# Kernel optimization log

Hardware: AMD Instinct MI355X
Metric: run time of the kernel (lower is better)

The kernel has to match this reference:

```python
import jax, jax.numpy as jnp
import numpy as np

H = 1024
B = 8192

def setup_inputs() -> dict:
    key = jax.random.key(0)
    ks = jax.random.split(key, 8)
    s = 1.0 / np.sqrt(H)
    return {
        "x": jax.random.normal(ks[0], (B, H), jnp.float32),
        "h": jax.random.normal(ks[1], (B, H), jnp.float32),
        "W_ih_w": jax.random.normal(ks[2], (3 * H, H), jnp.float32) * s,
        "W_ih_b": jax.random.normal(ks[3], (3 * H,), jnp.float32) * s,
        "U_r_w": jax.random.normal(ks[4], (H, H), jnp.float32) * s,
        "U_z_w": jax.random.normal(ks[5], (H, H), jnp.float32) * s,
        "U_n_w": jax.random.normal(ks[6], (H, H), jnp.float32) * s,
        "U_n_b": jax.random.normal(ks[7], (H,), jnp.float32) * s,
    }

def reference(x, h, W_ih_w, W_ih_b, U_r_w, U_z_w, U_n_w, U_n_b):
    # fused input projection: (B, 3H)
    x_proj = x @ W_ih_w.T + W_ih_b
    r_x, z_x, n_x = jnp.split(x_proj, 3, axis=-1)
    # per-gate hidden matmuls (transpose_U=False path)
    r_h = h @ U_r_w.T
    z_h = h @ U_z_w.T
    n_h = h @ U_n_w.T + U_n_b
    r = jax.nn.sigmoid(r_x + r_h)
    z = jax.nn.sigmoid(z_x + z_h)
    n = jnp.tanh(n_x + r * n_h)
    return (1.0 - z) * n + z * h
```

## Files before the change

kernel.cpp:

```cpp
#include <hip/hip_runtime.h>
#include <hip/hip_bf16.h>
#include <cstdint>

#define HDIM 1024
#define BM 128
#define BN 64
#define BKK 32

typedef __attribute__((ext_vector_type(8))) __bf16 bf16x8;
typedef __attribute__((ext_vector_type(8))) unsigned short u16x8;
typedef __attribute__((ext_vector_type(4))) float f32x4;

static __device__ __forceinline__ unsigned short f2b(float f) {
    __hip_bfloat16 h = __float2bfloat16(f);
    return __builtin_bit_cast(unsigned short, h);
}

__global__ void __launch_bounds__(256) cvt_kernel(const float* __restrict__ src,
                                                  unsigned short* __restrict__ dst,
                                                  int n4) {
    int i = blockIdx.x * blockDim.x + threadIdx.x;
    if (i >= n4) return;
    float4 v = ((const float4*)src)[i];
    ushort4 o;
    o.x = f2b(v.x); o.y = f2b(v.y); o.z = f2b(v.z); o.w = f2b(v.w);
    ((ushort4*)dst)[i] = o;
}

__global__ void __launch_bounds__(256, 2)
gru_fused(const float* __restrict__ xg, const float* __restrict__ hg,
          const unsigned short* __restrict__ wih,
          const unsigned short* __restrict__ ur,
          const unsigned short* __restrict__ uz,
          const unsigned short* __restrict__ un,
          const float* __restrict__ bih, const float* __restrict__ bun,
          float* __restrict__ out) {
    __shared__ __align__(16) unsigned short smem[20480];
    unsigned short* xs  = smem;
    unsigned short* hs  = smem + 4096;
    unsigned short* wsm = smem + 8192;

    const int tid  = threadIdx.x;
    const int lane = tid & 63;
    const int wv   = tid >> 6;
    const int wm   = wv >> 1;
    const int wn   = wv & 1;
    const int lr   = lane & 15;
    const int ls   = lane >> 4;
    const int m0   = blockIdx.y * BM;
    const int n0   = blockIdx.x * BN;

    const unsigned short* wb[6] = {
        wih + (size_t)n0 * HDIM,
        wih + (size_t)(HDIM + n0) * HDIM,
        wih + (size_t)(2 * HDIM + n0) * HDIM,
        ur  + (size_t)n0 * HDIM,
        uz  + (size_t)n0 * HDIM,
        un  + (size_t)n0 * HDIM
    };

    f32x4 acc[4][4][2];
#pragma unroll
    for (int g = 0; g < 4; ++g)
#pragma unroll
        for (int mf = 0; mf < 4; ++mf)
#pragma unroll
            for (int nf = 0; nf < 2; ++nf)
                acc[g][mf][nf] = f32x4{0.f, 0.f, 0.f, 0.f};

    for (int kt = 0; kt < HDIM / BKK; ++kt) {
        const int k0 = kt * BKK;

        {
            const int c  = wv * 64 + lane;
            const int r  = c >> 2;
            const int sl = c & 3;
#pragma unroll
            for (int mi = 0; mi < 6; ++mi) {
                const unsigned short* g = wb[mi] + (size_t)r * HDIM + k0 + sl * 8;
                unsigned short* l = wsm + mi * 2048 + wv * 512;
                __builtin_amdgcn_global_load_lds(
                    (const __attribute__((address_space(1))) void*)g,
                    (__attribute__((address_space(3))) void*)l, 16, 0, 0);
            }
        }

#pragma unroll
        for (int half = 0; half < 2; ++half) {
            const int ci = tid + half * 256;
            const int r  = ci >> 2;
            const int sl = ci & 3;
            const float* gx = xg + (size_t)(m0 + r) * HDIM + k0 + sl * 8;
            const float* gh = hg + (size_t)(m0 + r) * HDIM + k0 + sl * 8;
            float4 x0 = ((const float4*)gx)[0];
            float4 x1 = ((const float4*)gx)[1];
            float4 h0 = ((const float4*)gh)[0];
            float4 h1 = ((const float4*)gh)[1];
            u16x8 px, ph;
            px[0] = f2b(x0.x); px[1] = f2b(x0.y); px[2] = f2b(x0.z); px[3] = f2b(x0.w);
            px[4] = f2b(x1.x); px[5] = f2b(x1.y); px[6] = f2b(x1.z); px[7] = f2b(x1.w);
            ph[0] = f2b(h0.x); ph[1] = f2b(h0.y); ph[2] = f2b(h0.z); ph[3] = f2b(h0.w);
            ph[4] = f2b(h1.x); ph[5] = f2b(h1.y); ph[6] = f2b(h1.z); ph[7] = f2b(h1.w);
            *(u16x8*)(xs + ci * 8) = px;
            *(u16x8*)(hs + ci * 8) = ph;
        }

        __syncthreads();

        bf16x8 ax[4], ah[4];
#pragma unroll
        for (int mf = 0; mf < 4; ++mf) {
            ax[mf] = *(const bf16x8*)(xs + (wm * 64 + mf * 16 + lr) * 32 + ls * 8);
            ah[mf] = *(const bf16x8*)(hs + (wm * 64 + mf * 16 + lr) * 32 + ls * 8);
        }
#pragma unroll
        for (int mi = 0; mi < 6; ++mi) {
            const unsigned short* wt = wsm + mi * 2048;
            bf16x8 b0 = *(const bf16x8*)(wt + (wn * 32 + lr) * 32 + ls * 8);
            bf16x8 b1 = *(const bf16x8*)(wt + (wn * 32 + 16 + lr) * 32 + ls * 8);
            const int g = (mi == 0 || mi == 3) ? 0 : (mi == 1 || mi == 4) ? 1 : (mi == 2) ? 2 : 3;
            const bf16x8* a = (mi < 3) ? ax : ah;
#pragma unroll
            for (int mf = 0; mf < 4; ++mf) {
                acc[g][mf][0] = __builtin_amdgcn_mfma_f32_16x16x32_bf16(a[mf], b0, acc[g][mf][0], 0, 0, 0);
                acc[g][mf][1] = __builtin_amdgcn_mfma_f32_16x16x32_bf16(a[mf], b1, acc[g][mf][1], 0, 0, 0);
            }
        }
        __syncthreads();
    }

#pragma unroll
    for (int mf = 0; mf < 4; ++mf) {
#pragma unroll
        for (int nf = 0; nf < 2; ++nf) {
            const int gc = n0 + wn * 32 + nf * 16 + lr;
            const float br  = bih[gc];
            const float bz  = bih[HDIM + gc];
            const float bnx = bih[2 * HDIM + gc];
            const float bn2 = bun[gc];
            const f32x4 aR = acc[0][mf][nf];
            const f32x4 aZ = acc[1][mf][nf];
            const f32x4 aX = acc[2][mf][nf];
            const f32x4 aH = acc[3][mf][nf];
#pragma unroll
            for (int rr = 0; rr < 4; ++rr) {
                const int gr = m0 + wm * 64 + mf * 16 + ls * 4 + rr;
                const float rv = 1.f / (1.f + __expf(-(aR[rr] + br)));
                const float zv = 1.f / (1.f + __expf(-(aZ[rr] + bz)));
                const float nv = tanhf(aX[rr] + bnx + rv * (aH[rr] + bn2));
                const float hv = hg[(size_t)gr * HDIM + gc];
                out[(size_t)gr * HDIM + gc] = (1.f - zv) * nv + zv * hv;
            }
        }
    }
}

extern "C" void kernel_launch(void* const* d_in, const int* in_sizes, int n_in,
                              void* d_out, int out_size, void* d_ws, size_t ws_size,
                              hipStream_t stream) {
    const float* x   = (const float*)d_in[0];
    const float* h   = (const float*)d_in[1];
    const float* Wih = (const float*)d_in[2];
    const float* bih = (const float*)d_in[3];
    const float* Ur  = (const float*)d_in[4];
    const float* Uz  = (const float*)d_in[5];
    const float* Un  = (const float*)d_in[6];
    const float* bun = (const float*)d_in[7];
    float* out = (float*)d_out;

    unsigned short* wsp  = (unsigned short*)d_ws;
    unsigned short* wihb = wsp;
    unsigned short* urb  = wihb + 3 * 1024 * 1024;
    unsigned short* uzb  = urb + 1024 * 1024;
    unsigned short* unb  = uzb + 1024 * 1024;

    cvt_kernel<<<3072, 256, 0, stream>>>(Wih, wihb, 3 * 1024 * 1024 / 4);
    cvt_kernel<<<1024, 256, 0, stream>>>(Ur, urb, 1024 * 1024 / 4);
    cvt_kernel<<<1024, 256, 0, stream>>>(Uz, uzb, 1024 * 1024 / 4);
    cvt_kernel<<<1024, 256, 0, stream>>>(Un, unb, 1024 * 1024 / 4);

    dim3 grid(HDIM / BN, 8192 / BM);
    gru_fused<<<grid, 256, 0, stream>>>(x, h, wihb, urb, uzb, unb, bih, bun, out);
}
```

Before: 159.6 us.

## Double-buffer LDS tiles with XOR swizzle and pre-convert activations to bf16

```diff
diff --git a/kernel.cpp b/kernel.cpp
--- a/kernel.cpp
+++ b/kernel.cpp
@@ -6,6 +6,7 @@
 #define BM 128
 #define BN 64
 #define BKK 32
+#define NT (HDIM / BKK)
 
 typedef __attribute__((ext_vector_type(8))) __bf16 bf16x8;
 typedef __attribute__((ext_vector_type(8))) unsigned short u16x8;
@@ -16,29 +17,46 @@
     return __builtin_bit_cast(unsigned short, h);
 }
 
-__global__ void __launch_bounds__(256) cvt_kernel(const float* __restrict__ src,
-                                                  unsigned short* __restrict__ dst,
-                                                  int n4) {
-    int i = blockIdx.x * blockDim.x + threadIdx.x;
-    if (i >= n4) return;
+static __device__ __forceinline__ void barrier_fence() {
+    asm volatile("" ::: "memory");
+    __builtin_amdgcn_s_barrier();
+    asm volatile("" ::: "memory");
+}
+
+__global__ void __launch_bounds__(256) cvt_all(
+    const float* __restrict__ x, const float* __restrict__ h,
+    const float* __restrict__ wih, const float* __restrict__ ur,
+    const float* __restrict__ uz, const float* __restrict__ un,
+    unsigned short* __restrict__ wb, unsigned short* __restrict__ urb,
+    unsigned short* __restrict__ uzb, unsigned short* __restrict__ unb,
+    unsigned short* __restrict__ xb, unsigned short* __restrict__ hb) {
+    int b = blockIdx.x;
+    const float* src; unsigned short* dst; int idx;
+    if (b < 3072)       { src = wih; dst = wb;  idx = b; }
+    else if (b < 4096)  { src = ur;  dst = urb; idx = b - 3072; }
+    else if (b < 5120)  { src = uz;  dst = uzb; idx = b - 4096; }
+    else if (b < 6144)  { src = un;  dst = unb; idx = b - 5120; }
+    else if (b < 14336) { src = x;   dst = xb;  idx = b - 6144; }
+    else                { src = h;   dst = hb;  idx = b - 14336; }
+    int i = idx * 256 + threadIdx.x;
     float4 v = ((const float4*)src)[i];
     ushort4 o;
     o.x = f2b(v.x); o.y = f2b(v.y); o.z = f2b(v.z); o.w = f2b(v.w);
     ((ushort4*)dst)[i] = o;
 }
 
+template<bool XHB>
 __global__ void __launch_bounds__(256, 2)
-gru_fused(const float* __restrict__ xg, const float* __restrict__ hg,
+gru_fused(const float* __restrict__ hg,
+          const unsigned short* __restrict__ xb, const unsigned short* __restrict__ hb,
+          const float* __restrict__ xg32, const float* __restrict__ hg32,
           const unsigned short* __restrict__ wih,
           const unsigned short* __restrict__ ur,
           const unsigned short* __restrict__ uz,
           const unsigned short* __restrict__ un,
           const float* __restrict__ bih, const float* __restrict__ bun,
           float* __restrict__ out) {
-    __shared__ __align__(16) unsigned short smem[20480];
-    unsigned short* xs  = smem;
-    unsigned short* hs  = smem + 4096;
-    unsigned short* wsm = smem + 8192;
+    __shared__ __align__(16) unsigned short smem[2][20480];
 
     const int tid  = threadIdx.x;
     const int lane = tid & 63;
@@ -50,7 +68,7 @@
     const int m0   = blockIdx.y * BM;
     const int n0   = blockIdx.x * BN;
 
-    const unsigned short* wb[6] = {
+    const unsigned short* wb6[6] = {
         wih + (size_t)n0 * HDIM,
         wih + (size_t)(HDIM + n0) * HDIM,
         wih + (size_t)(2 * HDIM + n0) * HDIM,
@@ -59,6 +77,9 @@
         un  + (size_t)n0 * HDIM
     };
 
+    const int wr  = tid >> 2;
+    const int wsl = (tid & 3) ^ ((tid >> 3) & 3);
+
     f32x4 acc[4][4][2];
 #pragma unroll
     for (int g = 0; g < 4; ++g)
@@ -68,56 +89,85 @@
             for (int nf = 0; nf < 2; ++nf)
                 acc[g][mf][nf] = f32x4{0.f, 0.f, 0.f, 0.f};
 
-    for (int kt = 0; kt < HDIM / BKK; ++kt) {
+    auto STAGE = [&](int bufi, int kt) {
         const int k0 = kt * BKK;
-
-        {
-            const int c  = wv * 64 + lane;
-            const int r  = c >> 2;
-            const int sl = c & 3;
-#pragma unroll
-            for (int mi = 0; mi < 6; ++mi) {
-                const unsigned short* g = wb[mi] + (size_t)r * HDIM + k0 + sl * 8;
-                unsigned short* l = wsm + mi * 2048 + wv * 512;
+        unsigned short* sb = &smem[bufi][0];
+        float4 fx[2][2], fh[2][2];
+        if constexpr (!XHB) {
+#pragma unroll
+            for (int half = 0; half < 2; ++half) {
+                const int c2 = half * 256 + tid;
+                const int r2 = c2 >> 2;
+                const int sl = c2 & 3;
+                const float* gx = xg32 + (size_t)(m0 + r2) * HDIM + k0 + sl * 8;
+                const float* gh = hg32 + (size_t)(m0 + r2) * HDIM + k0 + sl * 8;
+                fx[half][0] = ((const float4*)gx)[0];
+                fx[half][1] = ((const float4*)gx)[1];
+                fh[half][0] = ((const float4*)gh)[0];
+                fh[half][1] = ((const float4*)gh)[1];
+            }
+        }
+#pragma unroll
+        for (int mi = 0; mi < 6; ++mi) {
+            const unsigned short* g = wb6[mi] + (size_t)wr * HDIM + k0 + wsl * 8;
+            __builtin_amdgcn_global_load_lds(
+                (const __attribute__((address_space(1))) void*)g,
+                (__attribute__((address_space(3))) void*)(sb + 8192 + mi * 2048 + wv * 512),
+                16, 0, 0);
+        }
+        if constexpr (XHB) {
+#pragma unroll
+            for (int half = 0; half < 2; ++half) {
+                const int c2 = half * 256 + tid;
+                const int r2 = c2 >> 2;
+                const int sl = (c2 & 3) ^ ((c2 >> 3) & 3);
+                const unsigned short* gx = xb + (size_t)(m0 + r2) * HDIM + k0 + sl * 8;
+                const unsigned short* gh = hb + (size_t)(m0 + r2) * HDIM + k0 + sl * 8;
                 __builtin_amdgcn_global_load_lds(
-                    (const __attribute__((address_space(1))) void*)g,
-                    (__attribute__((address_space(3))) void*)l, 16, 0, 0);
-            }
-        }
-
-#pragma unroll
-        for (int half = 0; half < 2; ++half) {
-            const int ci = tid + half * 256;
-            const int r  = ci >> 2;
-            const int sl = ci & 3;
-            const float* gx = xg + (size_t)(m0 + r) * HDIM + k0 + sl * 8;
-            const float* gh = hg + (size_t)(m0 + r) * HDIM + k0 + sl * 8;
-            float4 x0 = ((const float4*)gx)[0];
-            float4 x1 = ((const float4*)gx)[1];
-            float4 h0 = ((const float4*)gh)[0];
-            float4 h1 = ((const float4*)gh)[1];
-            u16x8 px, ph;
-            px[0] = f2b(x0.x); px[1] = f2b(x0.y); px[2] = f2b(x0.z); px[3] = f2b(x0.w);
-            px[4] = f2b(x1.x); px[5] = f2b(x1.y); px[6] = f2b(x1.z); px[7] = f2b(x1.w);
-            ph[0] = f2b(h0.x); ph[1] = f2b(h0.y); ph[2] = f2b(h0.z); ph[3] = f2b(h0.w);
-            ph[4] = f2b(h1.x); ph[5] = f2b(h1.y); ph[6] = f2b(h1.z); ph[7] = f2b(h1.w);
-            *(u16x8*)(xs + ci * 8) = px;
-            *(u16x8*)(hs + ci * 8) = ph;
-        }
-
-        __syncthreads();
-
+                    (const __attribute__((address_space(1))) void*)gx,
+                    (__attribute__((address_space(3))) void*)(sb + half * 2048 + wv * 512),
+                    16, 0, 0);
+                __builtin_amdgcn_global_load_lds(
+                    (const __attribute__((address_space(1))) void*)gh,
+                    (__attribute__((address_space(3))) void*)(sb + 4096 + half * 2048 + wv * 512),
+                    16, 0, 0);
+            }
+        } else {
+#pragma unroll
+            for (int half = 0; half < 2; ++half) {
+                const int c2 = half * 256 + tid;
+                const int r2 = c2 >> 2;
+                const int sp = (c2 & 3) ^ ((c2 >> 3) & 3);
+                u16x8 px, ph;
+#pragma unroll
+                for (int q = 0; q < 4; ++q) {
+                    px[q]     = f2b(fx[half][0][q]);
+                    px[q + 4] = f2b(fx[half][1][q]);
+                    ph[q]     = f2b(fh[half][0][q]);
+                    ph[q + 4] = f2b(fh[half][1][q]);
+                }
+                *(u16x8*)(sb + r2 * 32 + sp * 8)        = px;
+                *(u16x8*)(sb + 4096 + r2 * 32 + sp * 8) = ph;
+            }
+        }
+    };
+
+    auto COMPUTE = [&](int bufi) {
+        const unsigned short* sb = &smem[bufi][0];
+        const int sel = (lr >> 1) & 3;
+        const int fo  = (ls ^ sel) << 3;
         bf16x8 ax[4], ah[4];
 #pragma unroll
         for (int mf = 0; mf < 4; ++mf) {
-            ax[mf] = *(const bf16x8*)(xs + (wm * 64 + mf * 16 + lr) * 32 + ls * 8);
-            ah[mf] = *(const bf16x8*)(hs + (wm * 64 + mf * 16 + lr) * 32 + ls * 8);
+            const int row = wm * 64 + mf * 16 + lr;
+            ax[mf] = *(const bf16x8*)(sb + row * 32 + fo);
+            ah[mf] = *(const bf16x8*)(sb + 4096 + row * 32 + fo);
         }
 #pragma unroll
         for (int mi = 0; mi < 6; ++mi) {
-            const unsigned short* wt = wsm + mi * 2048;
-            bf16x8 b0 = *(const bf16x8*)(wt + (wn * 32 + lr) * 32 + ls * 8);
-            bf16x8 b1 = *(const bf16x8*)(wt + (wn * 32 + 16 + lr) * 32 + ls * 8);
+            const unsigned short* wt = sb + 8192 + mi * 2048;
+            bf16x8 b0 = *(const bf16x8*)(wt + (wn * 32 + lr) * 32 + fo);
+            bf16x8 b1 = *(const bf16x8*)(wt + (wn * 32 + 16 + lr) * 32 + fo);
             const int g = (mi == 0 || mi == 3) ? 0 : (mi == 1 || mi == 4) ? 1 : (mi == 2) ? 2 : 3;
             const bf16x8* a = (mi < 3) ? ax : ah;
 #pragma unroll
@@ -126,18 +176,37 @@
                 acc[g][mf][1] = __builtin_amdgcn_mfma_f32_16x16x32_bf16(a[mf], b1, acc[g][mf][1], 0, 0, 0);
             }
         }
-        __syncthreads();
+    };
+
+    auto WAITN = [&]() {
+        if constexpr (XHB) asm volatile("s_waitcnt vmcnt(10)" ::: "memory");
+        else               asm volatile("s_waitcnt vmcnt(6) lgkmcnt(0)" ::: "memory");
+    };
+
+    STAGE(0, 0);
+#pragma unroll 1
+    for (int kt = 0; kt < NT - 2; kt += 2) {
+        STAGE(1, kt + 1); WAITN(); barrier_fence();
+        COMPUTE(0);       barrier_fence();
+        STAGE(0, kt + 2); WAITN(); barrier_fence();
+        COMPUTE(1);       barrier_fence();
     }
-
-#pragma unroll
-    for (int mf = 0; mf < 4; ++mf) {
-#pragma unroll
-        for (int nf = 0; nf < 2; ++nf) {
-            const int gc = n0 + wn * 32 + nf * 16 + lr;
-            const float br  = bih[gc];
-            const float bz  = bih[HDIM + gc];
-            const float bnx = bih[2 * HDIM + gc];
-            const float bn2 = bun[gc];
+    STAGE(1, NT - 1); WAITN(); barrier_fence();
+    COMPUTE(0);       barrier_fence();
+    asm volatile("s_waitcnt vmcnt(0) lgkmcnt(0)" ::: "memory");
+    __builtin_amdgcn_s_barrier();
+    asm volatile("" ::: "memory");
+    COMPUTE(1);
+
+#pragma unroll
+    for (int nf = 0; nf < 2; ++nf) {
+        const int gc = n0 + wn * 32 + nf * 16 + lr;
+        const float br  = bih[gc];
+        const float bz  = bih[HDIM + gc];
+        const float bnx = bih[2 * HDIM + gc];
+        const float bn2 = bun[gc];
+#pragma unroll
+        for (int mf = 0; mf < 4; ++mf) {
             const f32x4 aR = acc[0][mf][nf];
             const f32x4 aZ = acc[1][mf][nf];
             const f32x4 aX = acc[2][mf][nf];
@@ -173,12 +242,19 @@
     unsigned short* urb  = wihb + 3 * 1024 * 1024;
     unsigned short* uzb  = urb + 1024 * 1024;
     unsigned short* unb  = uzb + 1024 * 1024;
-
-    cvt_kernel<<<3072, 256, 0, stream>>>(Wih, wihb, 3 * 1024 * 1024 / 4);
-    cvt_kernel<<<1024, 256, 0, stream>>>(Ur, urb, 1024 * 1024 / 4);
-    cvt_kernel<<<1024, 256, 0, stream>>>(Uz, uzb, 1024 * 1024 / 4);
-    cvt_kernel<<<1024, 256, 0, stream>>>(Un, unb, 1024 * 1024 / 4);
+    unsigned short* xb   = unb + 1024 * 1024;
+    unsigned short* hb   = xb + 8 * 1024 * 1024;
+
+    const bool xhb = ws_size >= 46137344ull;
+
+    cvt_all<<<xhb ? 22528 : 6144, 256, 0, stream>>>(
+        x, h, Wih, Ur, Uz, Un, wihb, urb, uzb, unb, xb, hb);
 
     dim3 grid(HDIM / BN, 8192 / BM);
-    gru_fused<<<grid, 256, 0, stream>>>(x, h, wihb, urb, uzb, unb, bih, bun, out);
-}
+    if (xhb)
+        gru_fused<true><<<grid, 256, 0, stream>>>(
+            h, xb, hb, nullptr, nullptr, wihb, urb, uzb, unb, bih, bun, out);
+    else
+        gru_fused<false><<<grid, 256, 0, stream>>>(
+            h, nullptr, nullptr, x, h, wihb, urb, uzb, unb, bih, bun, out);
+}
```

Result: faster. 142.4 us (-10.8%).
